# Kernel tuning notes

Hardware: AMD Instinct MI355X
Metric: run time of the kernel (lower is better)

The kernel has to match this reference:

```python
import jax, jax.numpy as jnp
import numpy as np

GAMMA = 1.0  # matches init_kwargs gamma
B, N, M = 128, 512, 512


def setup_inputs() -> dict:
    key = jax.random.key(0)
    D = jax.random.uniform(key, (B, N, M), dtype=jnp.float32)
    return {"D": D}


def _softmin3(a, b, c, gamma):
    # soft_min over the 3 DP neighbors: -gamma * logsumexp(-x/gamma)
    z = jnp.stack([a, b, c], axis=0) * (-1.0 / gamma)
    return -gamma * jax.nn.logsumexp(z, axis=0)


def reference(D):
    """Soft-DTW forward: returns R[:, N, M], shape (B,).
    DP over rows (lax.scan), inner scan over columns carries R[i, j-1].
    Vectorized over the batch dimension.
    """
    gamma = GAMMA
    b, n, m = D.shape
    dt = D.dtype
    inf = jnp.array(jnp.inf, dt)

    def row_step(prev_row, d_row):
        # prev_row: (b, m+1) = R[i-1, 0..m]; d_row: (b, m) = D[:, i-1, :]
        def col_step(left, xs):
            diag, up, d = xs  # each (b,)
            new = d + _softmin3(diag, up, left, gamma)
            return new, new
        xs = (prev_row[:, :-1].T, prev_row[:, 1:].T, d_row.T)  # each (m, b)
        _, outs = jax.lax.scan(col_step, jnp.full((b,), inf, dt), xs)
        new_row = jnp.concatenate([jnp.full((b, 1), inf, dt), outs.T], axis=1)
        return new_row, None

    # R[0, :] = [0, inf, inf, ...]
    init = jnp.concatenate([jnp.zeros((b, 1), dt), jnp.full((b, m), inf, dt)], axis=1)
    final_row, _ = jax.lax.scan(row_step, init, jnp.swapaxes(D, 0, 1))  # scan over rows (n, b, m)
    return final_row[:, -1]
```

## Files before the change

kernel.cpp:

```cpp
#include <hip/hip_runtime.h>


#define BB 128
#define NN 512
#define MM 512
#define L2E 1.4426950408889634f
#define LN2 0.6931471805599453f

typedef float f32x4 __attribute__((ext_vector_type(4)));

__device__ __forceinline__ int iclamp(int x, int lo, int hi) {
    return x < lo ? lo : (x > hi ? hi : x);
}

template<int CTRL>
__device__ __forceinline__ float dpp_fmax(float v) {
    const int s = __builtin_amdgcn_update_dpp(
        __float_as_int(v), __float_as_int(v), CTRL, 0xF, 0xF, false);
    return __builtin_fmaxf(v, __int_as_float(s));
}

__device__ __forceinline__ float dpp_shr1(float v) {
    const int s = __builtin_amdgcn_update_dpp(
        __float_as_int(v), __float_as_int(v), 0x138, 0xF, 0xF, false);
    return __int_as_float(s);
}

template<int T>
__device__ __forceinline__ void dostep(
    const float* __restrict__ Db, const int lane, const bool wpub,
    const int jb, const int sbase, const int tq,
    float (&r1)[4], float (&r2)[4], float4 (&buf)[16],
    int& irow, float& sh, float& shprev, float& bl, float& bd,
    const f32x4 (&bv)[4], const unsigned wrA)
{
    {
        const int r = iclamp(irow, 0, NN - 1);
        buf[(T + 8) & 15] = *(const float4*)(Db + ((r << 9) + jb));
        irow += 1;
    }
    const int s = sbase + T;

    float nv0, nv1, nv2, nv3;
    {
        constexpr int i3 = (16 + T - 3) & 15;
        const float d = buf[i3].w;
        float wg = __builtin_amdgcn_exp2f(-L2E * d);
        wg = ((s - 3) >= tq) ? 0.0f : wg;
        nv3 = wg * ((r1[3] + r1[2]) + r2[2]);
    }
    {
        constexpr int i2 = (16 + T - 2) & 15;
        const float d = buf[i2].z;
        float wg = __builtin_amdgcn_exp2f(-L2E * d);
        wg = ((s - 2) >= tq) ? 0.0f : wg;
        nv2 = wg * ((r1[2] + r1[1]) + r2[1]);
    }
    {
        constexpr int i1 = (16 + T - 1) & 15;
        const float d = buf[i1].y;
        float wg = __builtin_amdgcn_exp2f(-L2E * d);
        wg = ((s - 1) >= tq) ? 0.0f : wg;
        nv1 = wg * ((r1[1] + r1[0]) + r2[0]);
    }
    if (wpub)
        asm volatile("ds_write_b32 %0, %1 offset:%2"
                     :: "v"(wrA), "v"(nv3), "n"(T * 4));
    {
        constexpr int i0 = T & 15;
        const float d = buf[i0].x;
        const float lf = (lane == 0) ? bl : sh;
        const float dg = (lane == 0) ? bd : shprev;
        float wg = __builtin_amdgcn_exp2f(-L2E * d);
        wg = (s >= tq) ? 0.0f : wg;
        nv0 = wg * ((r1[0] + lf) + dg);
    }

    r2[0] = r1[0]; r2[1] = r1[1]; r2[2] = r1[2]; r2[3] = r1[3];
    r1[0] = nv0;   r1[1] = nv1;   r1[2] = nv2;   r1[3] = nv3;
    bd = bl;
    bl = bv[T >> 2][T & 3];
    shprev = sh;
    sh = dpp_shr1(nv3);
}

__device__ __forceinline__ void renorm_local(
    float (&r1)[4], float (&r2)[4], float& sh, float& shprev,
    float& bl, float& bd, float& gexp)
{
    float m = __builtin_fmaxf(__builtin_fmaxf(r1[0], r1[1]),
                              __builtin_fmaxf(r1[2], r1[3]));
    m = dpp_fmax<0x111>(m);
    m = dpp_fmax<0x112>(m);
    m = dpp_fmax<0x114>(m);
    m = dpp_fmax<0x118>(m);
    m = dpp_fmax<0x142>(m);
    m = dpp_fmax<0x143>(m);
    const int mb = __builtin_amdgcn_readlane(__float_as_int(m), 63);
    const int eb = (mb >> 23) & 255;
    const int ex = (eb > 0 && eb < 255) ? (eb - 127) : 0;
    const float rs = __int_as_float((127 - ex) << 23);
    r1[0] *= rs; r1[1] *= rs; r1[2] *= rs; r1[3] *= rs;
    r2[0] *= rs; r2[1] *= rs; r2[2] *= rs; r2[3] *= rs;
    sh *= rs; shprev *= rs;
    bl *= rs;
    bd *= rs;
    gexp += (float)ex;
}

#define DSTEP(T) dostep<T>(Db,lane,wpub,jb,sbase,tq,r1,r2,buf,irow,sh,shprev,bl,bd,bv,wrA);

__launch_bounds__(128, 1)
__global__ void softdtw_skew2(const float* __restrict__ D, float* __restrict__ out) {
    const int b = blockIdx.x;
    const int tid = (int)threadIdx.x;
    const int w = tid >> 6;
    const int lane = tid & 63;
    const int jb = (w << 8) + (lane << 2);
    const int tq = jb + NN;
    const bool wpub = (w == 0) && (lane == 63);
    const float* __restrict__ Db = D + (size_t)b * (NN * MM);

    __shared__ __align__(16) float ldsF[66];
    const unsigned ldsbase = (unsigned)(size_t)(void*)ldsF;
    const unsigned ringb = ldsbase;
    const unsigned gxb   = ldsbase + 256u;

    float r1[4] = {0.0f, 0.0f, 0.0f, 0.0f};
    float r2[4] = {0.0f, 0.0f, 0.0f, 0.0f};
    float4 buf[16];
    buf[13] = make_float4(0.f, 0.f, 0.f, 0.f);
    buf[14] = make_float4(0.f, 0.f, 0.f, 0.f);
    buf[15] = make_float4(0.f, 0.f, 0.f, 0.f);
    #pragma unroll
    for (int v = 0; v < 8; ++v) {
        const int r = iclamp(v - jb, 0, NN - 1);
        buf[v] = *(const float4*)(Db + ((r << 9) + jb));
    }
    int irow = 8 - jb;
    float sh = 0.0f, shprev = 0.0f;
    float bl = 0.0f;
    float bd = (w == 0) ? 1.0f : 0.0f;
    float gexp = 0.0f;

    #pragma unroll 1
    for (int k = 0; k < 65; ++k) {
        asm volatile("s_waitcnt lgkmcnt(0)\n\ts_barrier");
        const int kw = k - w;
        if (kw < 0 || kw > 63) continue;
        const int sbase = kw << 4;

        f32x4 q0, q1, q2, q3; float gxp;
        {
            const unsigned raddr = ringb + (((unsigned)sbase & 63u) << 2);
            const unsigned gaddr = gxb + (((unsigned)(k - 1) & 1u) << 2);
            asm volatile(
                "ds_read_b128 %0, %5\n\t"
                "ds_read_b128 %1, %5 offset:16\n\t"
                "ds_read_b128 %2, %5 offset:32\n\t"
                "ds_read_b128 %3, %5 offset:48\n\t"
                "ds_read_b32  %4, %6\n\t"
                "s_waitcnt lgkmcnt(0)"
                : "=&v"(q0), "=&v"(q1), "=&v"(q2), "=&v"(q3), "=&v"(gxp)
                : "v"(raddr), "v"(gaddr));
        }

        renorm_local(r1, r2, sh, shprev, bl, bd, gexp);

        if (wpub) {
            const unsigned ga = gxb + (((unsigned)k & 1u) << 2);
            asm volatile("ds_write_b32 %0, %1" :: "v"(ga), "v"(gexp));
        }

        float scale;
        {
            int dlt = (int)(gxp - gexp);
            dlt = iclamp(dlt, -126, 126);
            scale = __int_as_float((127 + dlt) << 23);
        }
        const bool act = (w > 0);
        const f32x4 zz = {0.0f, 0.0f, 0.0f, 0.0f};
        f32x4 bv[4];
        bv[0] = act ? q0 * scale : zz;
        bv[1] = act ? q1 * scale : zz;
        bv[2] = act ? q2 * scale : zz;
        bv[3] = act ? q3 * scale : zz;

        const unsigned wrA = ringb + (((unsigned)sbase & 63u) << 2);

        if (kw < 63) {
            DSTEP(0)  DSTEP(1)  DSTEP(2)  DSTEP(3)
            DSTEP(4)  DSTEP(5)  DSTEP(6)  DSTEP(7)
            DSTEP(8)  DSTEP(9)  DSTEP(10) DSTEP(11)
            DSTEP(12) DSTEP(13) DSTEP(14) DSTEP(15)
        } else {
            DSTEP(0)  DSTEP(1)  DSTEP(2)  DSTEP(3)
            DSTEP(4)  DSTEP(5)  DSTEP(6)  DSTEP(7)
            DSTEP(8)  DSTEP(9)  DSTEP(10) DSTEP(11)
            DSTEP(12) DSTEP(13) DSTEP(14)
        }
    }

    if (w == 1 && lane == 63) {
        out[b] = -(__builtin_amdgcn_logf(r1[3]) + gexp) * LN2;
    }
}

extern "C" void kernel_launch(void* const* d_in, const int* in_sizes, int n_in,
                              void* d_out, int out_size, void* d_ws, size_t ws_size,
                              hipStream_t stream) {
    const float* D = (const float*)d_in[0];
    float* out = (float*)d_out;
    softdtw_skew2<<<BB, 128, 0, stream>>>(D, out);
}
```

Before: 320.2 us.

## Stage D prefetch through per-lane LDS FIFO to deepen load lookahead

Replaces the 16-entry register ring of D rows with an 8-entry register buffer, 8 staging registers and a per-lane 16-entry LDS FIFO. Global loads are now issued about 11 or more steps ahead. Each value passes through LDS before reaching the compute buffer. This is meant to hide global-memory latency on the serial anti-diagonal recurrence, at the cost of extra LDS traffic (about 35 KB of shared memory) and a more involved prologue.

```diff
diff --git a/kernel.cpp b/kernel.cpp
--- a/kernel.cpp
+++ b/kernel.cpp
@@ -29,36 +29,35 @@
 template<int T>
 __device__ __forceinline__ void dostep(
     const float* __restrict__ Db, const int lane, const bool wpub,
-    const int jb, const int sbase, const int tq,
-    float (&r1)[4], float (&r2)[4], float4 (&buf)[16],
-    int& irow, float& sh, float& shprev, float& bl, float& bd,
+    const int jb, const int fj, const int fourb, const int sbase, const int tq,
+    float (&r1)[4], float (&r2)[4], float4 (&buf)[8], float4 (&stg)[8],
+    float4* fifoL,
+    float& sh, float& shprev, float& bl, float& bd,
     const f32x4 (&bv)[4], const unsigned wrA)
 {
-    {
-        const int r = iclamp(irow, 0, NN - 1);
-        buf[(T + 8) & 15] = *(const float4*)(Db + ((r << 9) + jb));
-        irow += 1;
-    }
     const int s = sbase + T;
-
-    float nv0, nv1, nv2, nv3;
-    {
-        constexpr int i3 = (16 + T - 3) & 15;
-        const float d = buf[i3].w;
+    fifoL[(T + 3 + fourb) & 15] = stg[T & 7];
+    {
+        const int row = iclamp((sbase + (T + 11)) + fj, 0, NN - 1);
+        stg[T & 7] = *(const float4*)(Db + ((row << 9) + jb));
+    }
+    buf[(T + 3) & 7] = fifoL[(T + 3) & 15];
+
+    float nv1, nv2, nv3;
+    {
+        const float d = buf[(T + 5) & 7].w;
         float wg = __builtin_amdgcn_exp2f(-L2E * d);
         wg = ((s - 3) >= tq) ? 0.0f : wg;
         nv3 = wg * ((r1[3] + r1[2]) + r2[2]);
     }
     {
-        constexpr int i2 = (16 + T - 2) & 15;
-        const float d = buf[i2].z;
+        const float d = buf[(T + 6) & 7].z;
         float wg = __builtin_amdgcn_exp2f(-L2E * d);
         wg = ((s - 2) >= tq) ? 0.0f : wg;
         nv2 = wg * ((r1[2] + r1[1]) + r2[1]);
     }
     {
-        constexpr int i1 = (16 + T - 1) & 15;
-        const float d = buf[i1].y;
+        const float d = buf[(T + 7) & 7].y;
         float wg = __builtin_amdgcn_exp2f(-L2E * d);
         wg = ((s - 1) >= tq) ? 0.0f : wg;
         nv1 = wg * ((r1[1] + r1[0]) + r2[0]);
@@ -66,9 +65,9 @@
     if (wpub)
         asm volatile("ds_write_b32 %0, %1 offset:%2"
                      :: "v"(wrA), "v"(nv3), "n"(T * 4));
-    {
-        constexpr int i0 = T & 15;
-        const float d = buf[i0].x;
+    float nv0;
+    {
+        const float d = buf[T & 7].x;
         const float lf = (lane == 0) ? bl : sh;
         const float dg = (lane == 0) ? bd : shprev;
         float wg = __builtin_amdgcn_exp2f(-L2E * d);
@@ -108,36 +107,63 @@
     gexp += (float)ex;
 }
 
-#define DSTEP(T) dostep<T>(Db,lane,wpub,jb,sbase,tq,r1,r2,buf,irow,sh,shprev,bl,bd,bv,wrA);
+#define DSTEP(T) dostep<T>(Db,lane,wpub,jb,fj,fourb,sbase,tq,r1,r2,buf,stg,fifoL,sh,shprev,bl,bd,bv,wrA);
 
 __launch_bounds__(128, 1)
-__global__ void softdtw_skew2(const float* __restrict__ D, float* __restrict__ out) {
+__global__ void softdtw_stg(const float* __restrict__ D, float* __restrict__ out) {
     const int b = blockIdx.x;
     const int tid = (int)threadIdx.x;
     const int w = tid >> 6;
     const int lane = tid & 63;
     const int jb = (w << 8) + (lane << 2);
+    const int fourb = (lane & 3) << 2;
+    const int fj = fourb - jb;
     const int tq = jb + NN;
     const bool wpub = (w == 0) && (lane == 63);
     const float* __restrict__ Db = D + (size_t)b * (NN * MM);
 
+    __shared__ float4 fifoS[2][64][17];
     __shared__ __align__(16) float ldsF[66];
+    float4* fifoL = &fifoS[w][lane][0];
     const unsigned ldsbase = (unsigned)(size_t)(void*)ldsF;
     const unsigned ringb = ldsbase;
     const unsigned gxb   = ldsbase + 256u;
 
     float r1[4] = {0.0f, 0.0f, 0.0f, 0.0f};
     float r2[4] = {0.0f, 0.0f, 0.0f, 0.0f};
-    float4 buf[16];
-    buf[13] = make_float4(0.f, 0.f, 0.f, 0.f);
-    buf[14] = make_float4(0.f, 0.f, 0.f, 0.f);
-    buf[15] = make_float4(0.f, 0.f, 0.f, 0.f);
+    float4 buf[8];
+    float4 stg[8];
     #pragma unroll
-    for (int v = 0; v < 8; ++v) {
-        const int r = iclamp(v - jb, 0, NN - 1);
-        buf[v] = *(const float4*)(Db + ((r << 9) + jb));
-    }
-    int irow = 8 - jb;
+    for (int i = 0; i < 8; ++i) buf[i] = make_float4(0.f, 0.f, 0.f, 0.f);
+
+    {
+        float4 pb[8];
+        #pragma unroll
+        for (int e = 3; e < 11; ++e) {
+            const int row = iclamp(e - jb, 0, NN - 1);
+            pb[e - 3] = *(const float4*)(Db + ((row << 9) + jb));
+        }
+        #pragma unroll
+        for (int e = 3; e < 11; ++e) fifoL[e & 15] = pb[e - 3];
+        #pragma unroll
+        for (int e = 11; e < 19; ++e) {
+            const int row = iclamp(e - jb, 0, NN - 1);
+            pb[e - 11] = *(const float4*)(Db + ((row << 9) + jb));
+        }
+        #pragma unroll
+        for (int e = 11; e < 19; ++e) fifoL[e & 15] = pb[e - 11];
+    }
+    #pragma unroll
+    for (int j = 0; j < 8; ++j) {
+        const int row = iclamp((j + 3) + fj, 0, NN - 1);
+        stg[j] = *(const float4*)(Db + ((row << 9) + jb));
+    }
+    #pragma unroll
+    for (int e = 0; e < 3; ++e) {
+        const int row = iclamp(e - jb, 0, NN - 1);
+        buf[e] = *(const float4*)(Db + ((row << 9) + jb));
+    }
+
     float sh = 0.0f, shprev = 0.0f;
     float bl = 0.0f;
     float bd = (w == 0) ? 1.0f : 0.0f;
@@ -211,5 +237,5 @@
                               hipStream_t stream) {
     const float* D = (const float*)d_in[0];
     float* out = (float*)d_out;
-    softdtw_skew2<<<BB, 128, 0, stream>>>(D, out);
-}
+    softdtw_stg<<<BB, 128, 0, stream>>>(D, out);
+}
```

Measured after the change: 647.5 us. +102.2%, slower.
